# Kernel optimization log

Hardware: AMD Instinct MI355X
Metric: run time of the kernel (lower is better)

The kernel has to match this reference:

```python
import jax, jax.numpy as jnp
import numpy as np

B, N, V = 8, 2000, 2000
K = 100            # local_size
EMB = 128          # ff_hidden_dim
PENALTY = -1e9
EPS = 1e-5         # InstanceNorm eps


def setup_inputs() -> dict:
    key = jax.random.key(0)
    ks = jax.random.split(key, 16)
    s = 0.02
    return {
        "dist": jax.random.uniform(ks[0], (B, N, V), dtype=jnp.float32),
        "theta": jax.random.normal(ks[1], (B, N, V), dtype=jnp.float32),
        "scale": jax.random.uniform(ks[2], (B, N, 1), dtype=jnp.float32),
        # Linear params stored [in, out]
        "w1": jax.random.normal(ks[3], (2 * K + 1, EMB), dtype=jnp.float32) * s,
        "b1": jnp.zeros((EMB,), jnp.float32),
        "w2": jax.random.normal(ks[4], (EMB, 2 * EMB), dtype=jnp.float32) * s,
        "b2": jnp.zeros((2 * EMB,), jnp.float32),
        "w3": jax.random.normal(ks[5], (2 * EMB, EMB), dtype=jnp.float32) * s,
        "b3": jnp.zeros((EMB,), jnp.float32),
        "w4": jax.random.normal(ks[6], (EMB, K), dtype=jnp.float32) * s,
        "b4": jnp.zeros((K,), jnp.float32),
        "gamma": jnp.ones((2 * EMB,), jnp.float32),   # InstanceNorm affine weight
        "beta": jnp.zeros((2 * EMB,), jnp.float32),   # InstanceNorm affine bias
    }


def reference(dist, theta, scale, w1, b1, w2, b2, w3, b3, w4, b4, gamma, beta):
    # --- topk smallest distances (ascending) + gather theta ---
    neg_vals, idx = jax.lax.top_k(-dist, K)          # [B,N,K]
    sorted_dist = -neg_vals                           # ascending k smallest
    sorted_dist = sorted_dist / jnp.max(sorted_dist, axis=-1, keepdims=True)
    sorted_theta = jnp.take_along_axis(theta, idx, axis=-1)  # [B,N,K]

    # --- small MLP with InstanceNorm over the node dim ---
    x_in = jnp.concatenate([sorted_dist, sorted_theta, scale], axis=-1)  # [B,N,2K+1]
    emb = jax.nn.relu(x_in @ w1 + b1)                 # [B,N,EMB]
    h = jax.nn.relu(emb @ w2 + b2)                    # [B,N,2*EMB]
    # InstanceNorm1d: normalize each channel over the length (node) dim, biased var
    mean = jnp.mean(h, axis=1, keepdims=True)
    var = jnp.var(h, axis=1, keepdims=True)
    h = (h - mean) * jax.lax.rsqrt(var + EPS) * gamma + beta
    emb = jax.nn.relu(h @ w3 + b3)                    # [B,N,EMB]
    out = (emb @ w4 + b4) - sorted_dist               # [B,N,K]

    # --- scatter into penalty-initialized matrix ---
    out_mat = jnp.full((B, N, V), PENALTY, dtype=dist.dtype)
    b_ix = jnp.arange(B)[:, None, None]
    n_ix = jnp.arange(N)[None, :, None]
    return out_mat.at[b_ix, n_ix, idx].set(out)
```

## Files before the change

### kernel.cpp

```cpp
#include <hip/hip_runtime.h>
#include <hip/hip_bf16.h>

#define BB 8
#define NN 2000
#define VV 2000
#define KK 100
#define EMB 128
#define PENALTY -1e9f
#define NBIN 512
#define BINSCALE 2048.0f
#define CAP 200
#define XPAD 224
#define SMALLTHR (255.0f / 2048.0f)
#define NWPACK 212
#define TOPKB (BB * NN / 4)

typedef __attribute__((ext_vector_type(8))) short short8;
typedef __attribute__((ext_vector_type(4))) float f32x4;

#define WB() __builtin_amdgcn_wave_barrier()

__device__ __forceinline__ unsigned short bf16rne(float f) {
    unsigned u = __float_as_uint(f);
    u += 0x7FFF + ((u >> 16) & 1);
    return (unsigned short)(u >> 16);
}
__device__ __forceinline__ float bf2f(unsigned short s) {
    return __uint_as_float((unsigned)s << 16);
}

#define FORALL_VALS(BODY)                                                    \
    _Pragma("unroll") for (int ci = 0; ci < 8; ++ci) {                       \
        { const int j = 0; const float fv = v4[ci].x; const int e = (ci * 64 + lane) * 4 + 0; BODY } \
        { const int j = 1; const float fv = v4[ci].y; const int e = (ci * 64 + lane) * 4 + 1; BODY } \
        { const int j = 2; const float fv = v4[ci].z; const int e = (ci * 64 + lane) * 4 + 2; BODY } \
        { const int j = 3; const float fv = v4[ci].w; const int e = (ci * 64 + lane) * 4 + 3; BODY } \
    }

__global__ __launch_bounds__(256) void topk_kernel(
    const float* __restrict__ dist, const float* __restrict__ scale,
    unsigned short* __restrict__ xin, unsigned short* __restrict__ sdist,
    unsigned short* __restrict__ idxb,
    const float* __restrict__ w1, const float* __restrict__ w2,
    const float* __restrict__ w3, const float* __restrict__ w4,
    unsigned short* __restrict__ pw1, unsigned short* __restrict__ pw2,
    unsigned short* __restrict__ pw3, unsigned short* __restrict__ pw4)
{
    __shared__ __align__(16) unsigned hist[4][NBIN / 2];
    __shared__ __align__(16) unsigned snap[4][NBIN / 2];
    __shared__ unsigned long long comp[4][CAP];
    __shared__ unsigned long long comp2[4][KK];
    __shared__ int sh_cnt[4], sh_ntie[4], sh_kth[4];
    __shared__ unsigned sh_pref[4];
    __shared__ int sh_tie[4][64];

    const int t = threadIdx.x;

    if (blockIdx.x < NWPACK) {
        const int bt = blockIdx.x;
        for (int e = t; e < 512; e += 256) {
            int lane = e >> 3, j = e & 7;
            int kk = ((lane >> 4) << 3) + j;
            int nn = lane & 15;
            if (bt < 56) {
                int kt = bt >> 3, nt = bt & 7;
                int k = kt * 32 + kk, n = nt * 16 + nn;
                float f = (k < 201) ? w1[k * 128 + n] : 0.f;
                pw1[bt * 512 + e] = bf16rne(f);
            } else if (bt < 120) {
                int bb = bt - 56, kt = bb >> 4, nt = bb & 15;
                pw2[bb * 512 + e] = bf16rne(w2[(kt * 32 + kk) * 256 + nt * 16 + nn]);
            } else if (bt < 184) {
                int bb = bt - 120, kt = bb >> 3, nt = bb & 7;
                pw3[bb * 512 + e] = bf16rne(w3[(kt * 32 + kk) * 128 + nt * 16 + nn]);
            } else {
                int bb = bt - 184, kt = bb / 7, nt = bb % 7;
                int n = nt * 16 + nn;
                float f = (n < 100) ? w4[(kt * 32 + kk) * 100 + n] : 0.f;
                pw4[bb * 512 + e] = bf16rne(f);
            }
        }
        return;
    }

    const int w = t >> 6, lane = t & 63;
    const int row = (blockIdx.x - NWPACK) * 4 + w;
    const float4* d4 = (const float4*)(dist + (size_t)row * VV);

    float4 v4[8];
#pragma unroll
    for (int c = 0; c < 7; ++c) v4[c] = d4[c * 64 + lane];
    v4[7] = (lane < 52) ? d4[448 + lane] : make_float4(2.f, 2.f, 2.f, 2.f);

    int nsmall = 0;
    FORALL_VALS({ nsmall += (fv < SMALLTHR) ? 1 : 0; (void)e; (void)j; (void)ci; });
#pragma unroll
    for (int off = 1; off < 64; off <<= 1) nsmall += __shfl_xor(nsmall, off);
    const bool fast = (nsmall >= KK);

#pragma unroll
    for (int i = 0; i < 4; ++i) hist[w][lane * 4 + i] = 0u;
    if (lane == 0) { sh_cnt[w] = 0; sh_ntie[w] = 0; }
    WB();

    unsigned bcache[8];
    FORALL_VALS({
        int b = (int)(fv * BINSCALE);
        b = b < 0 ? 0 : (b > NBIN - 1 ? NBIN - 1 : b);
        int bb = b > 255 ? 255 : b;
        if (j == 0) bcache[ci] = (unsigned)bb;
        else bcache[ci] |= (unsigned)bb << (8 * j);
        bool doh = fast ? (b < 255) : (b < NBIN - 1);
        if (doh) atomicAdd(&hist[w][b >> 1], 1u << ((b & 1) << 4));
        (void)e;
    });
    WB();

    unsigned cw0 = hist[w][lane * 4 + 0];
    unsigned cw1 = hist[w][lane * 4 + 1];
    unsigned cw2 = hist[w][lane * 4 + 2];
    unsigned cw3 = hist[w][lane * 4 + 3];
    unsigned tot = (cw0 & 0xFFFFu) + (cw0 >> 16) + (cw1 & 0xFFFFu) + (cw1 >> 16) +
                   (cw2 & 0xFFFFu) + (cw2 >> 16) + (cw3 & 0xFFFFu) + (cw3 >> 16);
    unsigned incl = tot;
#pragma unroll
    for (int off = 1; off < 64; off <<= 1) {
        unsigned v = __shfl_up(incl, (unsigned)off);
        if (lane >= off) incl += v;
    }
    unsigned run = incl - tot;

    int myBt = -1, myM = 0;
#pragma unroll
    for (int i = 0; i < 4; ++i) {
        unsigned cwi = (i == 0) ? cw0 : (i == 1) ? cw1 : (i == 2) ? cw2 : cw3;
        unsigned c0 = cwi & 0xFFFFu, c1 = cwi >> 16;
        unsigned st0 = run, st1 = run + c0;
        if (myBt < 0 && st0 < KK && st0 + c0 >= KK) {
            myBt = lane * 8 + 2 * i; myM = (int)(st0 + c0);
        }
        if (myBt < 0 && st1 < KK && st1 + c1 >= KK) {
            myBt = lane * 8 + 2 * i + 1; myM = (int)(st1 + c1);
        }
        unsigned packed = st0 | (st1 << 16);
        hist[w][lane * 4 + i] = packed;
        snap[w][lane * 4 + i] = packed;
        run = st1 + c1;
    }
    WB();

    unsigned long long bl = __ballot(myBt >= 0);
    int Bt, m;
    if (bl != 0ull) {
        int src = __ffsll(bl) - 1;
        Bt = __shfl(myBt, src);
        m = __shfl(myM, src);
    } else {
        Bt = NBIN - 1;
        m = 100000;
    }

    if (m <= CAP) {
        FORALL_VALS({
            int b;
            if (fast) b = (int)((bcache[ci] >> (8 * j)) & 255u);
            else {
                b = (int)(fv * BINSCALE);
                b = b < 0 ? 0 : (b > NBIN - 1 ? NBIN - 1 : b);
            }
            if (b <= Bt) {
                int sh = (b & 1) << 4;
                unsigned old = atomicAdd(&hist[w][b >> 1], 1u << sh);
                int slot = (int)((old >> sh) & 0xFFFFu);
                comp[w][slot] =
                    ((unsigned long long)__float_as_uint(fv) << 32) | (unsigned)e;
            }
        });
        WB();
        for (int o = lane; o < m; o += 64) {
            unsigned long long key = comp[w][o];
            float fv = __uint_as_float((unsigned)(key >> 32));
            int b = (int)(fv * BINSCALE);
            b = b < 0 ? 0 : (b > NBIN - 1 ? NBIN - 1 : b);
            int sh = (b & 1) << 4;
            unsigned e0 = (hist[w][b >> 1] >> sh) & 0xFFFFu;
            unsigned s0 = (snap[w][b >> 1] >> sh) & 0xFFFFu;
            int r = (int)s0;
            for (unsigned s = s0; s < e0; ++s) r += (comp[w][s] < key);
            if (r < KK) comp2[w][r] = key;
        }
    } else {
        FORALL_VALS({
            int b = (int)(fv * BINSCALE);
            b = b < 0 ? 0 : (b > NBIN - 1 ? NBIN - 1 : b);
            if (b < Bt) {
                int pos = atomicAdd(&sh_cnt[w], 1);
                if (pos < CAP)
                    comp[w][pos] =
                        ((unsigned long long)__float_as_uint(fv) << 32) | (unsigned)e;
            }
            (void)j; (void)ci;
        });
        WB();
        int nless = sh_cnt[w];
        if (lane == 0) { sh_pref[w] = 0u; sh_kth[w] = KK - nless; }
        WB();
        for (int p = 0; p < 4; ++p) {
#pragma unroll
            for (int i = 0; i < 4; ++i) hist[w][lane * 4 + i] = 0u;
            WB();
            const int shift = 24 - 8 * p;
            const unsigned pref = sh_pref[w];
            FORALL_VALS({
                int b = (int)(fv * BINSCALE);
                b = b < 0 ? 0 : (b > NBIN - 1 ? NBIN - 1 : b);
                if (b == Bt) {
                    unsigned k = __float_as_uint(fv);
                    bool ok = (p == 0) || ((k >> (shift + 8)) == pref);
                    if (ok) atomicAdd(&hist[w][(k >> shift) & 255u], 1u);
                }
                (void)e; (void)j; (void)ci;
            });
            WB();
            if (lane == 0) {
                int kth = sh_kth[w];
                unsigned cum = 0;
                int b = 0;
                for (; b < 256; ++b) {
                    unsigned cc = hist[w][b];
                    if (cum + cc >= (unsigned)kth) break;
                    cum += cc;
                }
                sh_pref[w] = (pref << 8) | (unsigned)b;
                sh_kth[w] = kth - (int)cum;
            }
            WB();
        }
        const unsigned T = sh_pref[w];
        const int need2 = sh_kth[w];
        FORALL_VALS({
            int b = (int)(fv * BINSCALE);
            b = b < 0 ? 0 : (b > NBIN - 1 ? NBIN - 1 : b);
            if (b == Bt) {
                unsigned k = __float_as_uint(fv);
                if (k < T) {
                    int pos = atomicAdd(&sh_cnt[w], 1);
                    if (pos < CAP)
                        comp[w][pos] = ((unsigned long long)k << 32) | (unsigned)e;
                } else if (k == T) {
                    int q = atomicAdd(&sh_ntie[w], 1);
                    if (q < 64) sh_tie[w][q] = e;
                }
            }
            (void)j; (void)ci;
        });
        WB();
        if (lane == 0) {
            int nl2 = sh_cnt[w];
            int nt = sh_ntie[w] < 64 ? sh_ntie[w] : 64;
            for (int i = 1; i < nt; ++i) {
                int v = sh_tie[w][i], j2 = i - 1;
                while (j2 >= 0 && sh_tie[w][j2] > v) {
                    sh_tie[w][j2 + 1] = sh_tie[w][j2];
                    --j2;
                }
                sh_tie[w][j2 + 1] = v;
            }
            for (int i = 0; i < need2; ++i)
                comp[w][nl2 + i] =
                    ((unsigned long long)T << 32) | (unsigned)sh_tie[w][i];
            sh_cnt[w] = nl2 + need2;
        }
        WB();
        const int mm = sh_cnt[w];
        for (int o = lane; o < mm; o += 64) {
            unsigned long long key = comp[w][o];
            int r = 0;
            for (int j2 = 0; j2 < mm; ++j2) {
                unsigned long long cj = comp[w][j2];
                r += (cj < key) || (cj == key && j2 < o);
            }
            if (r < KK) comp2[w][r] = key;
        }
    }
    WB();

    const float Tf = __uint_as_float((unsigned)(comp2[w][KK - 1] >> 32));
    const float invT = 1.0f / Tf;
    for (int o = lane; o < KK; o += 64) {
        unsigned long long c = comp2[w][o];
        unsigned kbits = (unsigned)(c >> 32);
        int id = (int)(c & 0xFFFFFFFFu);
        unsigned short nb = bf16rne(__uint_as_float(kbits) * invT);
        xin[(size_t)row * XPAD + o] = nb;
        sdist[(size_t)row * KK + o] = nb;
        idxb[(size_t)row * KK + o] = (unsigned short)id;
    }
    if (lane == 0) xin[(size_t)row * XPAD + 200] = bf16rne(scale[row]);
    else if (lane < 24) xin[(size_t)row * XPAD + 200 + lane] = 0;
}

__global__ __launch_bounds__(256) void gather_kernel(
    const float* __restrict__ theta, const unsigned short* __restrict__ idxb,
    unsigned short* __restrict__ xin)
{
    const int i = blockIdx.x * 256 + threadIdx.x;
    const int row = i / KK;
    const int k = i - row * KK;
    const int id = (int)idxb[i];
    float v = theta[(size_t)row * VV + id];
    xin[(size_t)row * XPAD + 100 + k] = bf16rne(v);
}

__global__ __launch_bounds__(256) void fused12_mfma(
    const unsigned short* __restrict__ xin, const unsigned short* __restrict__ pw1,
    const float* __restrict__ b1, const unsigned short* __restrict__ pw2,
    const float* __restrict__ b2, unsigned short* __restrict__ h)
{
    __shared__ unsigned short c1s[64][136];
    const int t = threadIdx.x;
    const int w = t >> 6, l = t & 63;
    const int m0 = blockIdx.x * 64;
    const int lr = l & 15, lg = l >> 4;

    f32x4 acc[8] = {};
    const short8* arow = (const short8*)(xin + (size_t)(m0 + 16 * w + lr) * XPAD);
    const short8* pw1v = (const short8*)pw1;
#pragma unroll
    for (int kt = 0; kt < 7; ++kt) {
        short8 a = arow[kt * 4 + lg];
#pragma unroll
        for (int nt = 0; nt < 8; ++nt) {
            short8 b = pw1v[(kt * 8 + nt) * 64 + l];
            acc[nt] = __builtin_amdgcn_mfma_f32_16x16x32_bf16(a, b, acc[nt], 0, 0, 0);
        }
    }
#pragma unroll
    for (int nt = 0; nt < 8; ++nt) {
        int col = nt * 16 + lr;
        float bb = b1[col];
#pragma unroll
        for (int r = 0; r < 4; ++r) {
            float v = fmaxf(acc[nt][r] + bb, 0.f);
            c1s[16 * w + lg * 4 + r][col] = bf16rne(v);
        }
    }
    __syncthreads();

    f32x4 acc2[16] = {};
    const short8* pw2v = (const short8*)pw2;
#pragma unroll
    for (int kt = 0; kt < 4; ++kt) {
        short8 a = *(const short8*)&c1s[16 * w + lr][kt * 32 + lg * 8];
#pragma unroll
        for (int nt = 0; nt < 16; ++nt) {
            short8 b = pw2v[(kt * 16 + nt) * 64 + l];
            acc2[nt] = __builtin_amdgcn_mfma_f32_16x16x32_bf16(a, b, acc2[nt], 0, 0, 0);
        }
    }
#pragma unroll
    for (int nt = 0; nt < 16; ++nt) {
        int col = nt * 16 + lr;
        float bb = b2[col];
#pragma unroll
        for (int r = 0; r < 4; ++r) {
            float v = fmaxf(acc2[nt][r] + bb, 0.f);
            h[(size_t)(m0 + 16 * w + lg * 4 + r) * 256 + col] = bf16rne(v);
        }
    }
}

#define NCHUNK 25
#define CHUNK (NN / NCHUNK)

__global__ __launch_bounds__(256) void stats_partial(
    const unsigned short* __restrict__ h, float* __restrict__ part)
{
    const int b = blockIdx.x, ch = blockIdx.y, c = threadIdx.x;
    const unsigned short* base = h + ((size_t)b * NN + (size_t)ch * CHUNK) * 256 + c;
    float s = 0.f, s2 = 0.f;
    for (int n = 0; n < CHUNK; ++n) {
        float v = bf2f(base[(size_t)n * 256]);
        s += v;
        s2 += v * v;
    }
    size_t o = (((size_t)b * NCHUNK + ch) * 256 + c) * 2;
    part[o] = s;
    part[o + 1] = s2;
}

__global__ __launch_bounds__(256) void stats_final(
    const float* __restrict__ part, const float* __restrict__ gamma,
    const float* __restrict__ beta, float* __restrict__ scv,
    float* __restrict__ shv)
{
    const int b = blockIdx.x, c = threadIdx.x;
    float s = 0.f, s2 = 0.f;
    for (int ch = 0; ch < NCHUNK; ++ch) {
        size_t o = (((size_t)b * NCHUNK + ch) * 256 + c) * 2;
        s += part[o];
        s2 += part[o + 1];
    }
    const float inv = 1.0f / (float)NN;
    float mean = s * inv;
    float var = s2 * inv - mean * mean;
    float rs = rsqrtf(var + 1e-5f);
    float sc = gamma[c] * rs;
    scv[b * 256 + c] = sc;
    shv[b * 256 + c] = beta[c] - mean * sc;
}

__global__ __launch_bounds__(256) void fused34_mfma(
    const unsigned short* __restrict__ h, const unsigned short* __restrict__ pw3,
    const float* __restrict__ b3, const unsigned short* __restrict__ pw4,
    const float* __restrict__ b4, const float* __restrict__ scv,
    const float* __restrict__ shv, const unsigned short* __restrict__ sdist,
    const unsigned short* __restrict__ idxb, float* __restrict__ out)
{
    __shared__ __align__(16) char uni[64 * 100 * 4];
    __shared__ __align__(16) unsigned bm[64][64];
    __shared__ __align__(16) unsigned short wpref[64][64];
    unsigned short (*c1s)[136] = (unsigned short (*)[136])uni;
    float (*valbuf)[100] = (float (*)[100])uni;

    const int t = threadIdx.x;
    const int w = t >> 6, l = t & 63;
    const int m0 = blockIdx.x * 64;
    const int lr = l & 15, lg = l >> 4;

    for (int i = t; i < 64 * 64; i += 256) ((unsigned*)bm)[i] = 0u;
    __syncthreads();

    for (int i = t; i < 64 * KK; i += 256) {
        int rrow = i / KK;
        int id = (int)idxb[(size_t)(m0 + rrow) * KK + (i - rrow * KK)];
        atomicOr(&bm[rrow][id >> 5], 1u << (id & 31));
    }

    const int myrow = m0 + 16 * w + lr;
    const int mybatch = myrow / NN;

    f32x4 acc[8] = {};
    const short8* hrow = (const short8*)(h + (size_t)myrow * 256);
    const short8* pw3v = (const short8*)pw3;
#pragma unroll
    for (int kt = 0; kt < 8; ++kt) {
        int k0 = kt * 32 + lg * 8;
        short8 hv = hrow[kt * 4 + lg];
        const float4* scp = (const float4*)(scv + mybatch * 256 + k0);
        const float4* shp = (const float4*)(shv + mybatch * 256 + k0);
        float4 sc0 = scp[0], sc1 = scp[1];
        float4 sh0 = shp[0], sh1 = shp[1];
        short8 a;
        a[0] = (short)bf16rne(fmaf(bf2f((unsigned short)hv[0]), sc0.x, sh0.x));
        a[1] = (short)bf16rne(fmaf(bf2f((unsigned short)hv[1]), sc0.y, sh0.y));
        a[2] = (short)bf16rne(fmaf(bf2f((unsigned short)hv[2]), sc0.z, sh0.z));
        a[3] = (short)bf16rne(fmaf(bf2f((unsigned short)hv[3]), sc0.w, sh0.w));
        a[4] = (short)bf16rne(fmaf(bf2f((unsigned short)hv[4]), sc1.x, sh1.x));
        a[5] = (short)bf16rne(fmaf(bf2f((unsigned short)hv[5]), sc1.y, sh1.y));
        a[6] = (short)bf16rne(fmaf(bf2f((unsigned short)hv[6]), sc1.z, sh1.z));
        a[7] = (short)bf16rne(fmaf(bf2f((unsigned short)hv[7]), sc1.w, sh1.w));
#pragma unroll
        for (int nt = 0; nt < 8; ++nt) {
            short8 b = pw3v[(kt * 8 + nt) * 64 + l];
            acc[nt] = __builtin_amdgcn_mfma_f32_16x16x32_bf16(a, b, acc[nt], 0, 0, 0);
        }
    }
    __syncthreads();

    if (t < 64) {
        unsigned run = 0;
#pragma unroll
        for (int wd = 0; wd < 63; ++wd) {
            wpref[t][wd] = (unsigned short)run;
            run += (unsigned)__popc(bm[t][wd]);
        }
        wpref[t][63] = (unsigned short)run;
    }

#pragma unroll
    for (int nt = 0; nt < 8; ++nt) {
        int col = nt * 16 + lr;
        float bb = b3[col];
#pragma unroll
        for (int r = 0; r < 4; ++r) {
            float v = fmaxf(acc[nt][r] + bb, 0.f);
            c1s[16 * w + lg * 4 + r][col] = bf16rne(v);
        }
    }
    __syncthreads();

    f32x4 acc2[7] = {};
    const short8* pw4v = (const short8*)pw4;
#pragma unroll
    for (int kt = 0; kt < 4; ++kt) {
        short8 a = *(const short8*)&c1s[16 * w + lr][kt * 32 + lg * 8];
#pragma unroll
        for (int nt = 0; nt < 7; ++nt) {
            short8 b = pw4v[(kt * 7 + nt) * 64 + l];
            acc2[nt] = __builtin_amdgcn_mfma_f32_16x16x32_bf16(a, b, acc2[nt], 0, 0, 0);
        }
    }
    __syncthreads();

#pragma unroll
    for (int nt = 0; nt < 7; ++nt) {
        int col = nt * 16 + lr;
        if (col < KK) {
            float bb = b4[col];
#pragma unroll
            for (int r = 0; r < 4; ++r) {
                int r4 = 16 * w + lg * 4 + r;
                int mrow = m0 + r4;
                float v = acc2[nt][r] + bb -
                          bf2f(sdist[(size_t)mrow * KK + col]);
                int id = (int)idxb[(size_t)mrow * KK + col];
                int wd = id >> 5;
                int irank = (int)wpref[r4][wd] +
                            __popc(bm[r4][wd] & ((1u << (id & 31)) - 1u));
                valbuf[r4][irank] = v;
            }
        }
    }
    __syncthreads();

    for (int i = t; i < 64 * (VV / 4); i += 256) {
        int rrow = i / (VV / 4);
        int p = i - rrow * (VV / 4);
        int v0 = p * 4;
        unsigned word = bm[rrow][v0 >> 5];
        int sh = v0 & 31;
        int racc = (int)wpref[rrow][v0 >> 5] + __popc(word & ((1u << sh) - 1u));
        float4 o;
        unsigned b0 = (word >> sh) & 1u;
        o.x = b0 ? valbuf[rrow][racc] : PENALTY; racc += b0;
        unsigned b1_ = (word >> (sh + 1)) & 1u;
        o.y = b1_ ? valbuf[rrow][racc] : PENALTY; racc += b1_;
        unsigned b2_ = (word >> (sh + 2)) & 1u;
        o.z = b2_ ? valbuf[rrow][racc] : PENALTY; racc += b2_;
        unsigned b3_ = (word >> (sh + 3)) & 1u;
        o.w = b3_ ? valbuf[rrow][racc] : PENALTY;
        ((float4*)(out + (size_t)(m0 + rrow) * VV))[p] = o;
    }
}

extern "C" void kernel_launch(void* const* d_in, const int* in_sizes, int n_in,
                              void* d_out, int out_size, void* d_ws, size_t ws_size,
                              hipStream_t stream)
{
    const float* dist  = (const float*)d_in[0];
    const float* theta = (const float*)d_in[1];
    const float* scale = (const float*)d_in[2];
    const float* w1 = (const float*)d_in[3];
    const float* b1 = (const float*)d_in[4];
    const float* w2 = (const float*)d_in[5];
    const float* b2 = (const float*)d_in[6];
    const float* w3 = (const float*)d_in[7];
    const float* b3 = (const float*)d_in[8];
    const float* w4 = (const float*)d_in[9];
    const float* b4 = (const float*)d_in[10];
    const float* gamma = (const float*)d_in[11];
    const float* beta  = (const float*)d_in[12];
    float* out = (float*)d_out;

    const int M = BB * NN;

    char* p = (char*)d_ws;
    unsigned short* xin   = (unsigned short*)p;     p += (size_t)M * XPAD * 2;
    unsigned short* h     = (unsigned short*)p;     p += (size_t)M * 256 * 2;
    unsigned short* sdist = (unsigned short*)p;     p += (size_t)M * KK * 2;
    unsigned short* idxb  = (unsigned short*)p;     p += (size_t)M * KK * 2;
    float* part  = (float*)p;                       p += (size_t)BB * NCHUNK * 256 * 2 * 4;
    float* scv   = (float*)p;                       p += 8 * 256 * 4;
    float* shv   = (float*)p;                       p += 8 * 256 * 4;
    unsigned short* pw1 = (unsigned short*)p;       p += 56 * 512 * 2;
    unsigned short* pw2 = (unsigned short*)p;       p += 64 * 512 * 2;
    unsigned short* pw3 = (unsigned short*)p;       p += 64 * 512 * 2;
    unsigned short* pw4 = (unsigned short*)p;       p += 28 * 512 * 2;

    topk_kernel<<<NWPACK + TOPKB, 256, 0, stream>>>(
        dist, scale, xin, sdist, idxb,
        w1, w2, w3, w4, pw1, pw2, pw3, pw4);

    gather_kernel<<<(M * KK) / 256, 256, 0, stream>>>(theta, idxb, xin);

    fused12_mfma<<<M / 64, 256, 0, stream>>>(xin, pw1, b1, pw2, b2, h);

    stats_partial<<<dim3(BB, NCHUNK), 256, 0, stream>>>(h, part);
    stats_final<<<BB, 256, 0, stream>>>(part, gamma, beta, scv, shv);

    fused34_mfma<<<M / 64, 256, 0, stream>>>(h, pw3, b3, pw4, b4, scv, shv,
                                             sdist, idxb, out);
}
```

Baseline: 133.8 us.

## Split each top-k row across two waves with block-level synchronization

The top-k selection kernel now assigns two wavefronts per row (two rows per block) instead of one wave per row. This halves the per-thread register footprint of the distance values and doubles the number of blocks. The cost is that wave barriers become full __syncthreads and the histogram is built via atomics from two waves. The fallback path is now taken by both rows together if either needs it, and the prefix scan runs on only half the threads.

```diff
diff --git a/kernel.cpp b/kernel.cpp
--- a/kernel.cpp
+++ b/kernel.cpp
@@ -13,12 +13,10 @@
 #define XPAD 224
 #define SMALLTHR (255.0f / 2048.0f)
 #define NWPACK 212
-#define TOPKB (BB * NN / 4)
+#define TOPKB (BB * NN / 2)
 
 typedef __attribute__((ext_vector_type(8))) short short8;
 typedef __attribute__((ext_vector_type(4))) float f32x4;
-
-#define WB() __builtin_amdgcn_wave_barrier()
 
 __device__ __forceinline__ unsigned short bf16rne(float f) {
     unsigned u = __float_as_uint(f);
@@ -29,12 +27,12 @@
     return __uint_as_float((unsigned)s << 16);
 }
 
-#define FORALL_VALS(BODY)                                                    \
-    _Pragma("unroll") for (int ci = 0; ci < 8; ++ci) {                       \
-        { const int j = 0; const float fv = v4[ci].x; const int e = (ci * 64 + lane) * 4 + 0; BODY } \
-        { const int j = 1; const float fv = v4[ci].y; const int e = (ci * 64 + lane) * 4 + 1; BODY } \
-        { const int j = 2; const float fv = v4[ci].z; const int e = (ci * 64 + lane) * 4 + 2; BODY } \
-        { const int j = 3; const float fv = v4[ci].w; const int e = (ci * 64 + lane) * 4 + 3; BODY } \
+#define FORALL16(BODY)                                                       \
+    _Pragma("unroll") for (int ci = 0; ci < 4; ++ci) {                       \
+        { const int j = 0; const float fv = v4[ci].x; const int e = (ci * 128 + hl) * 4 + 0; BODY } \
+        { const int j = 1; const float fv = v4[ci].y; const int e = (ci * 128 + hl) * 4 + 1; BODY } \
+        { const int j = 2; const float fv = v4[ci].z; const int e = (ci * 128 + hl) * 4 + 2; BODY } \
+        { const int j = 3; const float fv = v4[ci].w; const int e = (ci * 128 + hl) * 4 + 3; BODY } \
     }
 
 __global__ __launch_bounds__(256) void topk_kernel(
@@ -46,13 +44,15 @@
     unsigned short* __restrict__ pw1, unsigned short* __restrict__ pw2,
     unsigned short* __restrict__ pw3, unsigned short* __restrict__ pw4)
 {
-    __shared__ __align__(16) unsigned hist[4][NBIN / 2];
-    __shared__ __align__(16) unsigned snap[4][NBIN / 2];
-    __shared__ unsigned long long comp[4][CAP];
-    __shared__ unsigned long long comp2[4][KK];
-    __shared__ int sh_cnt[4], sh_ntie[4], sh_kth[4];
-    __shared__ unsigned sh_pref[4];
-    __shared__ int sh_tie[4][64];
+    __shared__ __align__(16) unsigned hist[2][NBIN / 2];
+    __shared__ __align__(16) unsigned snap[2][NBIN / 2];
+    __shared__ unsigned long long comp[2][CAP];
+    __shared__ unsigned long long comp2[2][KK];
+    __shared__ int sh_ns[2][2];
+    __shared__ int sh_Bt[2], sh_m[2];
+    __shared__ int sh_cnt[2], sh_ntie[2], sh_kth[2];
+    __shared__ unsigned sh_pref[2];
+    __shared__ int sh_tie[2][64];
 
     const int t = threadIdx.x;
 
@@ -84,84 +84,90 @@
     }
 
     const int w = t >> 6, lane = t & 63;
-    const int row = (blockIdx.x - NWPACK) * 4 + w;
+    const int wr = w >> 1;
+    const int half = w & 1;
+    const int hl = (half << 6) | lane;
+    const int row = (blockIdx.x - NWPACK) * 2 + wr;
     const float4* d4 = (const float4*)(dist + (size_t)row * VV);
 
-    float4 v4[8];
-#pragma unroll
-    for (int c = 0; c < 7; ++c) v4[c] = d4[c * 64 + lane];
-    v4[7] = (lane < 52) ? d4[448 + lane] : make_float4(2.f, 2.f, 2.f, 2.f);
+    float4 v4[4];
+#pragma unroll
+    for (int c = 0; c < 4; ++c) {
+        int i4 = c * 128 + hl;
+        v4[c] = (i4 < VV / 4) ? d4[i4] : make_float4(2.f, 2.f, 2.f, 2.f);
+    }
 
     int nsmall = 0;
-    FORALL_VALS({ nsmall += (fv < SMALLTHR) ? 1 : 0; (void)e; (void)j; (void)ci; });
-#pragma unroll
-    for (int off = 1; off < 64; off <<= 1) nsmall += __shfl_xor(nsmall, off);
-    const bool fast = (nsmall >= KK);
-
-#pragma unroll
-    for (int i = 0; i < 4; ++i) hist[w][lane * 4 + i] = 0u;
-    if (lane == 0) { sh_cnt[w] = 0; sh_ntie[w] = 0; }
-    WB();
-
-    unsigned bcache[8];
-    FORALL_VALS({
+    unsigned bcache[4];
+    FORALL16({
         int b = (int)(fv * BINSCALE);
         b = b < 0 ? 0 : (b > NBIN - 1 ? NBIN - 1 : b);
         int bb = b > 255 ? 255 : b;
         if (j == 0) bcache[ci] = (unsigned)bb;
         else bcache[ci] |= (unsigned)bb << (8 * j);
-        bool doh = fast ? (b < 255) : (b < NBIN - 1);
-        if (doh) atomicAdd(&hist[w][b >> 1], 1u << ((b & 1) << 4));
+        nsmall += (fv < SMALLTHR) ? 1 : 0;
         (void)e;
     });
-    WB();
-
-    unsigned cw0 = hist[w][lane * 4 + 0];
-    unsigned cw1 = hist[w][lane * 4 + 1];
-    unsigned cw2 = hist[w][lane * 4 + 2];
-    unsigned cw3 = hist[w][lane * 4 + 3];
-    unsigned tot = (cw0 & 0xFFFFu) + (cw0 >> 16) + (cw1 & 0xFFFFu) + (cw1 >> 16) +
-                   (cw2 & 0xFFFFu) + (cw2 >> 16) + (cw3 & 0xFFFFu) + (cw3 >> 16);
-    unsigned incl = tot;
-#pragma unroll
-    for (int off = 1; off < 64; off <<= 1) {
-        unsigned v = __shfl_up(incl, (unsigned)off);
-        if (lane >= off) incl += v;
-    }
-    unsigned run = incl - tot;
-
-    int myBt = -1, myM = 0;
-#pragma unroll
-    for (int i = 0; i < 4; ++i) {
-        unsigned cwi = (i == 0) ? cw0 : (i == 1) ? cw1 : (i == 2) ? cw2 : cw3;
-        unsigned c0 = cwi & 0xFFFFu, c1 = cwi >> 16;
-        unsigned st0 = run, st1 = run + c0;
-        if (myBt < 0 && st0 < KK && st0 + c0 >= KK) {
-            myBt = lane * 8 + 2 * i; myM = (int)(st0 + c0);
-        }
-        if (myBt < 0 && st1 < KK && st1 + c1 >= KK) {
-            myBt = lane * 8 + 2 * i + 1; myM = (int)(st1 + c1);
-        }
-        unsigned packed = st0 | (st1 << 16);
-        hist[w][lane * 4 + i] = packed;
-        snap[w][lane * 4 + i] = packed;
-        run = st1 + c1;
-    }
-    WB();
-
-    unsigned long long bl = __ballot(myBt >= 0);
-    int Bt, m;
-    if (bl != 0ull) {
-        int src = __ffsll(bl) - 1;
-        Bt = __shfl(myBt, src);
-        m = __shfl(myM, src);
-    } else {
-        Bt = NBIN - 1;
-        m = 100000;
-    }
-
-    if (m <= CAP) {
-        FORALL_VALS({
+#pragma unroll
+    for (int off = 1; off < 64; off <<= 1) nsmall += __shfl_xor(nsmall, off);
+
+    ((unsigned*)hist)[t] = 0u;
+    ((unsigned*)hist)[t + 256] = 0u;
+    if (lane == 0) sh_ns[wr][half] = nsmall;
+    if (t < 2) { sh_Bt[t] = NBIN - 1; sh_m[t] = 100000; sh_cnt[t] = 0; sh_ntie[t] = 0; }
+    __syncthreads();
+    const bool fast = (sh_ns[wr][0] + sh_ns[wr][1] >= KK);
+
+    FORALL16({
+        int b = (int)(fv * BINSCALE);
+        b = b < 0 ? 0 : (b > NBIN - 1 ? NBIN - 1 : b);
+        bool doh = fast ? (b < 255) : (b < NBIN - 1);
+        if (doh) atomicAdd(&hist[wr][b >> 1], 1u << ((b & 1) << 4));
+        (void)e; (void)j; (void)ci;
+    });
+    __syncthreads();
+
+    if (half == 0) {
+        unsigned cw0 = hist[wr][lane * 4 + 0];
+        unsigned cw1 = hist[wr][lane * 4 + 1];
+        unsigned cw2 = hist[wr][lane * 4 + 2];
+        unsigned cw3 = hist[wr][lane * 4 + 3];
+        unsigned tot = (cw0 & 0xFFFFu) + (cw0 >> 16) + (cw1 & 0xFFFFu) + (cw1 >> 16) +
+                       (cw2 & 0xFFFFu) + (cw2 >> 16) + (cw3 & 0xFFFFu) + (cw3 >> 16);
+        unsigned incl = tot;
+#pragma unroll
+        for (int off = 1; off < 64; off <<= 1) {
+            unsigned v = __shfl_up(incl, (unsigned)off);
+            if (lane >= off) incl += v;
+        }
+        unsigned run = incl - tot;
+
+        int myBt = -1, myM = 0;
+#pragma unroll
+        for (int i = 0; i < 4; ++i) {
+            unsigned cwi = (i == 0) ? cw0 : (i == 1) ? cw1 : (i == 2) ? cw2 : cw3;
+            unsigned c0 = cwi & 0xFFFFu, c1 = cwi >> 16;
+            unsigned st0 = run, st1 = run + c0;
+            if (myBt < 0 && st0 < KK && st0 + c0 >= KK) {
+                myBt = lane * 8 + 2 * i; myM = (int)(st0 + c0);
+            }
+            if (myBt < 0 && st1 < KK && st1 + c1 >= KK) {
+                myBt = lane * 8 + 2 * i + 1; myM = (int)(st1 + c1);
+            }
+            unsigned packed = st0 | (st1 << 16);
+            hist[wr][lane * 4 + i] = packed;
+            snap[wr][lane * 4 + i] = packed;
+            run = st1 + c1;
+        }
+        if (myBt >= 0) { sh_Bt[wr] = myBt; sh_m[wr] = myM; }
+    }
+    __syncthreads();
+    const int Bt = sh_Bt[wr];
+    const int m = sh_m[wr];
+    const bool anyfb = (sh_m[0] > CAP) || (sh_m[1] > CAP);
+
+    if (!anyfb) {
+        FORALL16({
             int b;
             if (fast) b = (int)((bcache[ci] >> (8 * j)) & 255u);
             else {
@@ -170,134 +176,134 @@
             }
             if (b <= Bt) {
                 int sh = (b & 1) << 4;
-                unsigned old = atomicAdd(&hist[w][b >> 1], 1u << sh);
+                unsigned old = atomicAdd(&hist[wr][b >> 1], 1u << sh);
                 int slot = (int)((old >> sh) & 0xFFFFu);
-                comp[w][slot] =
+                comp[wr][slot] =
                     ((unsigned long long)__float_as_uint(fv) << 32) | (unsigned)e;
             }
         });
-        WB();
-        for (int o = lane; o < m; o += 64) {
-            unsigned long long key = comp[w][o];
+        __syncthreads();
+        for (int o = hl; o < m; o += 128) {
+            unsigned long long key = comp[wr][o];
             float fv = __uint_as_float((unsigned)(key >> 32));
             int b = (int)(fv * BINSCALE);
             b = b < 0 ? 0 : (b > NBIN - 1 ? NBIN - 1 : b);
             int sh = (b & 1) << 4;
-            unsigned e0 = (hist[w][b >> 1] >> sh) & 0xFFFFu;
-            unsigned s0 = (snap[w][b >> 1] >> sh) & 0xFFFFu;
+            unsigned e0 = (hist[wr][b >> 1] >> sh) & 0xFFFFu;
+            unsigned s0 = (snap[wr][b >> 1] >> sh) & 0xFFFFu;
             int r = (int)s0;
-            for (unsigned s = s0; s < e0; ++s) r += (comp[w][s] < key);
-            if (r < KK) comp2[w][r] = key;
+            for (unsigned s = s0; s < e0; ++s) r += (comp[wr][s] < key);
+            if (r < KK) comp2[wr][r] = key;
         }
     } else {
-        FORALL_VALS({
+        FORALL16({
             int b = (int)(fv * BINSCALE);
             b = b < 0 ? 0 : (b > NBIN - 1 ? NBIN - 1 : b);
             if (b < Bt) {
-                int pos = atomicAdd(&sh_cnt[w], 1);
+                int pos = atomicAdd(&sh_cnt[wr], 1);
                 if (pos < CAP)
-                    comp[w][pos] =
+                    comp[wr][pos] =
                         ((unsigned long long)__float_as_uint(fv) << 32) | (unsigned)e;
             }
             (void)j; (void)ci;
         });
-        WB();
-        int nless = sh_cnt[w];
-        if (lane == 0) { sh_pref[w] = 0u; sh_kth[w] = KK - nless; }
-        WB();
+        __syncthreads();
+        int nless = sh_cnt[wr];
+        if (hl == 0) { sh_pref[wr] = 0u; sh_kth[wr] = KK - nless; }
+        __syncthreads();
         for (int p = 0; p < 4; ++p) {
-#pragma unroll
-            for (int i = 0; i < 4; ++i) hist[w][lane * 4 + i] = 0u;
-            WB();
+            hist[wr][hl] = 0u;
+            hist[wr][hl + 128] = 0u;
+            __syncthreads();
             const int shift = 24 - 8 * p;
-            const unsigned pref = sh_pref[w];
-            FORALL_VALS({
+            const unsigned pref = sh_pref[wr];
+            FORALL16({
                 int b = (int)(fv * BINSCALE);
                 b = b < 0 ? 0 : (b > NBIN - 1 ? NBIN - 1 : b);
                 if (b == Bt) {
                     unsigned k = __float_as_uint(fv);
                     bool ok = (p == 0) || ((k >> (shift + 8)) == pref);
-                    if (ok) atomicAdd(&hist[w][(k >> shift) & 255u], 1u);
+                    if (ok) atomicAdd(&hist[wr][(k >> shift) & 255u], 1u);
                 }
                 (void)e; (void)j; (void)ci;
             });
-            WB();
-            if (lane == 0) {
-                int kth = sh_kth[w];
+            __syncthreads();
+            if (hl == 0) {
+                int kth = sh_kth[wr];
                 unsigned cum = 0;
                 int b = 0;
                 for (; b < 256; ++b) {
-                    unsigned cc = hist[w][b];
+                    unsigned cc = hist[wr][b];
                     if (cum + cc >= (unsigned)kth) break;
                     cum += cc;
                 }
-                sh_pref[w] = (pref << 8) | (unsigned)b;
-                sh_kth[w] = kth - (int)cum;
-            }
-            WB();
-        }
-        const unsigned T = sh_pref[w];
-        const int need2 = sh_kth[w];
-        FORALL_VALS({
+                sh_pref[wr] = (pref << 8) | (unsigned)b;
+                sh_kth[wr] = kth - (int)cum;
+            }
+            __syncthreads();
+        }
+        const unsigned T = sh_pref[wr];
+        const int need2 = sh_kth[wr];
+        FORALL16({
             int b = (int)(fv * BINSCALE);
             b = b < 0 ? 0 : (b > NBIN - 1 ? NBIN - 1 : b);
             if (b == Bt) {
                 unsigned k = __float_as_uint(fv);
                 if (k < T) {
-                    int pos = atomicAdd(&sh_cnt[w], 1);
+                    int pos = atomicAdd(&sh_cnt[wr], 1);
                     if (pos < CAP)
-                        comp[w][pos] = ((unsigned long long)k << 32) | (unsigned)e;
+                        comp[wr][pos] = ((unsigned long long)k << 32) | (unsigned)e;
                 } else if (k == T) {
-                    int q = atomicAdd(&sh_ntie[w], 1);
-                    if (q < 64) sh_tie[w][q] = e;
+                    int q = atomicAdd(&sh_ntie[wr], 1);
+                    if (q < 64) sh_tie[wr][q] = e;
                 }
             }
             (void)j; (void)ci;
         });
-        WB();
-        if (lane == 0) {
-            int nl2 = sh_cnt[w];
-            int nt = sh_ntie[w] < 64 ? sh_ntie[w] : 64;
+        __syncthreads();
+        if (hl == 0) {
+            int nl2 = sh_cnt[wr];
+            int nt = sh_ntie[wr] < 64 ? sh_ntie[wr] : 64;
             for (int i = 1; i < nt; ++i) {
-                int v = sh_tie[w][i], j2 = i - 1;
-                while (j2 >= 0 && sh_tie[w][j2] > v) {
-                    sh_tie[w][j2 + 1] = sh_tie[w][j2];
+                int v = sh_tie[wr][i], j2 = i - 1;
+                while (j2 >= 0 && sh_tie[wr][j2] > v) {
+                    sh_tie[wr][j2 + 1] = sh_tie[wr][j2];
                     --j2;
                 }
-                sh_tie[w][j2 + 1] = v;
+                sh_tie[wr][j2 + 1] = v;
             }
             for (int i = 0; i < need2; ++i)
-                comp[w][nl2 + i] =
-                    ((unsigned long long)T << 32) | (unsigned)sh_tie[w][i];
-            sh_cnt[w] = nl2 + need2;
-        }
-        WB();
-        const int mm = sh_cnt[w];
-        for (int o = lane; o < mm; o += 64) {
-            unsigned long long key = comp[w][o];
+                comp[wr][nl2 + i] =
+                    ((unsigned long long)T << 32) | (unsigned)sh_tie[wr][i];
+            sh_cnt[wr] = nl2 + need2;
+        }
+        __syncthreads();
+        const int mm = sh_cnt[wr];
+        for (int o = hl; o < mm; o += 128) {
+            unsigned long long key = comp[wr][o];
             int r = 0;
             for (int j2 = 0; j2 < mm; ++j2) {
-                unsigned long long cj = comp[w][j2];
+                unsigned long long cj = comp[wr][j2];
                 r += (cj < key) || (cj == key && j2 < o);
             }
-            if (r < KK) comp2[w][r] = key;
-        }
-    }
-    WB();
-
-    const float Tf = __uint_as_float((unsigned)(comp2[w][KK - 1] >> 32));
+            if (r < KK) comp2[wr][r] = key;
+        }
+    }
+    __syncthreads();
+
+    const float Tf = __uint_as_float((unsigned)(comp2[wr][KK - 1] >> 32));
     const float invT = 1.0f / Tf;
-    for (int o = lane; o < KK; o += 64) {
-        unsigned long long c = comp2[w][o];
+    if (hl < KK) {
+        unsigned long long c = comp2[wr][hl];
         unsigned kbits = (unsigned)(c >> 32);
         int id = (int)(c & 0xFFFFFFFFu);
         unsigned short nb = bf16rne(__uint_as_float(kbits) * invT);
-        xin[(size_t)row * XPAD + o] = nb;
-        sdist[(size_t)row * KK + o] = nb;
-        idxb[(size_t)row * KK + o] = (unsigned short)id;
-    }
-    if (lane == 0) xin[(size_t)row * XPAD + 200] = bf16rne(scale[row]);
-    else if (lane < 24) xin[(size_t)row * XPAD + 200 + lane] = 0;
+        xin[(size_t)row * XPAD + hl] = nb;
+        sdist[(size_t)row * KK + hl] = nb;
+        idxb[(size_t)row * KK + hl] = (unsigned short)id;
+    }
+    if (hl == 0) xin[(size_t)row * XPAD + 200] = bf16rne(scale[row]);
+    else if (hl < 24) xin[(size_t)row * XPAD + 200 + hl] = 0;
 }
 
 __global__ __launch_bounds__(256) void gather_kernel(
```

Result: slower. 136.6 us (+2.1%).

## Fuse InstanceNorm statistics into layer-2 epilogue and finalize in layer-3 kernel

Applied to the files above, without the earlier changes.

Each fused12 block reduces its tile's per-channel sum and sum of squares in shared memory. It then atomically adds them into a small per-batch global buffer, which is zeroed by the topk kernel. This removes the stats_partial and stats_final launches and the re-read of h. fused34 now computes scale and shift from the raw sums at block start, handling tiles that straddle a batch boundary. In exchange it adds float atomics, which make the accumulation order nondeterministic, plus some redundant per-block rsqrt work.

```diff
diff --git a/kernel.cpp b/kernel.cpp
--- a/kernel.cpp
+++ b/kernel.cpp
@@ -44,7 +44,8 @@
     const float* __restrict__ w1, const float* __restrict__ w2,
     const float* __restrict__ w3, const float* __restrict__ w4,
     unsigned short* __restrict__ pw1, unsigned short* __restrict__ pw2,
-    unsigned short* __restrict__ pw3, unsigned short* __restrict__ pw4)
+    unsigned short* __restrict__ pw3, unsigned short* __restrict__ pw4,
+    float* __restrict__ part)
 {
     __shared__ __align__(16) unsigned hist[4][NBIN / 2];
     __shared__ __align__(16) unsigned snap[4][NBIN / 2];
@@ -58,6 +59,10 @@
 
     if (blockIdx.x < NWPACK) {
         const int bt = blockIdx.x;
+        if (bt == 0) {
+#pragma unroll
+            for (int i = 0; i < 16; ++i) part[i * 256 + t] = 0.f;
+        }
         for (int e = t; e < 512; e += 256) {
             int lane = e >> 3, j = e & 7;
             int kk = ((lane >> 4) << 3) + j;
@@ -315,9 +320,10 @@
 __global__ __launch_bounds__(256) void fused12_mfma(
     const unsigned short* __restrict__ xin, const unsigned short* __restrict__ pw1,
     const float* __restrict__ b1, const unsigned short* __restrict__ pw2,
-    const float* __restrict__ b2, unsigned short* __restrict__ h)
+    const float* __restrict__ b2, unsigned short* __restrict__ h,
+    float* __restrict__ part)
 {
-    __shared__ unsigned short c1s[64][136];
+    __shared__ __align__(16) unsigned short c1s[64][136];
     const int t = threadIdx.x;
     const int w = t >> 6, l = t & 63;
     const int m0 = blockIdx.x * 64;
@@ -358,63 +364,49 @@
             acc2[nt] = __builtin_amdgcn_mfma_f32_16x16x32_bf16(a, b, acc2[nt], 0, 0, 0);
         }
     }
+    __syncthreads();
+    float* sums = (float*)c1s;
+    for (int i = t; i < 1024; i += 256) sums[i] = 0.f;
+    __syncthreads();
+
+    const int batch0 = m0 / NN;
+    const int bl = ((m0 + 16 * w + lg * 4) / NN) - batch0;
 #pragma unroll
     for (int nt = 0; nt < 16; ++nt) {
         int col = nt * 16 + lr;
         float bb = b2[col];
+        float s = 0.f, s2 = 0.f;
 #pragma unroll
         for (int r = 0; r < 4; ++r) {
             float v = fmaxf(acc2[nt][r] + bb, 0.f);
             h[(size_t)(m0 + 16 * w + lg * 4 + r) * 256 + col] = bf16rne(v);
-        }
-    }
-}
-
-#define NCHUNK 25
-#define CHUNK (NN / NCHUNK)
-
-__global__ __launch_bounds__(256) void stats_partial(
-    const unsigned short* __restrict__ h, float* __restrict__ part)
-{
-    const int b = blockIdx.x, ch = blockIdx.y, c = threadIdx.x;
-    const unsigned short* base = h + ((size_t)b * NN + (size_t)ch * CHUNK) * 256 + c;
-    float s = 0.f, s2 = 0.f;
-    for (int n = 0; n < CHUNK; ++n) {
-        float v = bf2f(base[(size_t)n * 256]);
-        s += v;
-        s2 += v * v;
-    }
-    size_t o = (((size_t)b * NCHUNK + ch) * 256 + c) * 2;
-    part[o] = s;
-    part[o + 1] = s2;
-}
-
-__global__ __launch_bounds__(256) void stats_final(
-    const float* __restrict__ part, const float* __restrict__ gamma,
-    const float* __restrict__ beta, float* __restrict__ scv,
-    float* __restrict__ shv)
-{
-    const int b = blockIdx.x, c = threadIdx.x;
-    float s = 0.f, s2 = 0.f;
-    for (int ch = 0; ch < NCHUNK; ++ch) {
-        size_t o = (((size_t)b * NCHUNK + ch) * 256 + c) * 2;
-        s += part[o];
-        s2 += part[o + 1];
-    }
-    const float inv = 1.0f / (float)NN;
-    float mean = s * inv;
-    float var = s2 * inv - mean * mean;
-    float rs = rsqrtf(var + 1e-5f);
-    float sc = gamma[c] * rs;
-    scv[b * 256 + c] = sc;
-    shv[b * 256 + c] = beta[c] - mean * sc;
+            s += v;
+            s2 += v * v;
+        }
+        atomicAdd(&sums[(bl * 256 + col) * 2 + 0], s);
+        atomicAdd(&sums[(bl * 256 + col) * 2 + 1], s2);
+    }
+    __syncthreads();
+    {
+        const int col = t;
+        const bool strad = ((m0 + 63) / NN) != batch0;
+        atomicAdd(&part[(batch0 * 256 + col) * 2 + 0], sums[col * 2 + 0]);
+        atomicAdd(&part[(batch0 * 256 + col) * 2 + 1], sums[col * 2 + 1]);
+        if (strad) {
+            atomicAdd(&part[((batch0 + 1) * 256 + col) * 2 + 0],
+                      sums[(256 + col) * 2 + 0]);
+            atomicAdd(&part[((batch0 + 1) * 256 + col) * 2 + 1],
+                      sums[(256 + col) * 2 + 1]);
+        }
+    }
 }
 
 __global__ __launch_bounds__(256) void fused34_mfma(
     const unsigned short* __restrict__ h, const unsigned short* __restrict__ pw3,
     const float* __restrict__ b3, const unsigned short* __restrict__ pw4,
-    const float* __restrict__ b4, const float* __restrict__ scv,
-    const float* __restrict__ shv, const unsigned short* __restrict__ sdist,
+    const float* __restrict__ b4, const float* __restrict__ part,
+    const float* __restrict__ gamma, const float* __restrict__ beta,
+    const unsigned short* __restrict__ sdist,
     const unsigned short* __restrict__ idxb, float* __restrict__ out)
 {
     __shared__ __align__(16) char uni[64 * 100 * 4];
@@ -422,11 +414,36 @@
     __shared__ __align__(16) unsigned short wpref[64][64];
     unsigned short (*c1s)[136] = (unsigned short (*)[136])uni;
     float (*valbuf)[100] = (float (*)[100])uni;
+    float* scl = (float*)wpref;
+    float* shl = scl + 512;
 
     const int t = threadIdx.x;
     const int w = t >> 6, l = t & 63;
     const int m0 = blockIdx.x * 64;
     const int lr = l & 15, lg = l >> 4;
+    const int batch0 = m0 / NN;
+    const bool strad = ((m0 + 63) / NN) != batch0;
+
+    {
+        const int col = t;
+        float g = gamma[col], be = beta[col];
+        float s = part[(batch0 * 256 + col) * 2 + 0];
+        float s2 = part[(batch0 * 256 + col) * 2 + 1];
+        float mean = s * (1.0f / NN);
+        float var = s2 * (1.0f / NN) - mean * mean;
+        float sc = g * rsqrtf(var + 1e-5f);
+        scl[col] = sc;
+        shl[col] = be - mean * sc;
+        if (strad) {
+            s = part[((batch0 + 1) * 256 + col) * 2 + 0];
+            s2 = part[((batch0 + 1) * 256 + col) * 2 + 1];
+            mean = s * (1.0f / NN);
+            var = s2 * (1.0f / NN) - mean * mean;
+            sc = g * rsqrtf(var + 1e-5f);
+            scl[256 + col] = sc;
+            shl[256 + col] = be - mean * sc;
+        }
+    }
 
     for (int i = t; i < 64 * 64; i += 256) ((unsigned*)bm)[i] = 0u;
     __syncthreads();
@@ -438,7 +455,8 @@
     }
 
     const int myrow = m0 + 16 * w + lr;
-    const int mybatch = myrow / NN;
+    const int bl = (myrow / NN) - batch0;
+    const int nbase = bl * 256;
 
     f32x4 acc[8] = {};
     const short8* hrow = (const short8*)(h + (size_t)myrow * 256);
@@ -447,19 +465,11 @@
     for (int kt = 0; kt < 8; ++kt) {
         int k0 = kt * 32 + lg * 8;
         short8 hv = hrow[kt * 4 + lg];
-        const float4* scp = (const float4*)(scv + mybatch * 256 + k0);
-        const float4* shp = (const float4*)(shv + mybatch * 256 + k0);
-        float4 sc0 = scp[0], sc1 = scp[1];
-        float4 sh0 = shp[0], sh1 = shp[1];
         short8 a;
-        a[0] = (short)bf16rne(fmaf(bf2f((unsigned short)hv[0]), sc0.x, sh0.x));
-        a[1] = (short)bf16rne(fmaf(bf2f((unsigned short)hv[1]), sc0.y, sh0.y));
-        a[2] = (short)bf16rne(fmaf(bf2f((unsigned short)hv[2]), sc0.z, sh0.z));
-        a[3] = (short)bf16rne(fmaf(bf2f((unsigned short)hv[3]), sc0.w, sh0.w));
-        a[4] = (short)bf16rne(fmaf(bf2f((unsigned short)hv[4]), sc1.x, sh1.x));
-        a[5] = (short)bf16rne(fmaf(bf2f((unsigned short)hv[5]), sc1.y, sh1.y));
-        a[6] = (short)bf16rne(fmaf(bf2f((unsigned short)hv[6]), sc1.z, sh1.z));
-        a[7] = (short)bf16rne(fmaf(bf2f((unsigned short)hv[7]), sc1.w, sh1.w));
+#pragma unroll
+        for (int i = 0; i < 8; ++i)
+            a[i] = (short)bf16rne(fmaf(bf2f((unsigned short)hv[i]),
+                                       scl[nbase + k0 + i], shl[nbase + k0 + i]));
 #pragma unroll
         for (int nt = 0; nt < 8; ++nt) {
             short8 b = pw3v[(kt * 8 + nt) * 64 + l];
@@ -570,9 +580,7 @@
     unsigned short* h     = (unsigned short*)p;     p += (size_t)M * 256 * 2;
     unsigned short* sdist = (unsigned short*)p;     p += (size_t)M * KK * 2;
     unsigned short* idxb  = (unsigned short*)p;     p += (size_t)M * KK * 2;
-    float* part  = (float*)p;                       p += (size_t)BB * NCHUNK * 256 * 2 * 4;
-    float* scv   = (float*)p;                       p += 8 * 256 * 4;
-    float* shv   = (float*)p;                       p += 8 * 256 * 4;
+    float* part  = (float*)p;                       p += 8 * 256 * 2 * 4;
     unsigned short* pw1 = (unsigned short*)p;       p += 56 * 512 * 2;
     unsigned short* pw2 = (unsigned short*)p;       p += 64 * 512 * 2;
     unsigned short* pw3 = (unsigned short*)p;       p += 64 * 512 * 2;
@@ -580,15 +588,12 @@
 
     topk_kernel<<<NWPACK + TOPKB, 256, 0, stream>>>(
         dist, scale, xin, sdist, idxb,
-        w1, w2, w3, w4, pw1, pw2, pw3, pw4);
+        w1, w2, w3, w4, pw1, pw2, pw3, pw4, part);
 
     gather_kernel<<<(M * KK) / 256, 256, 0, stream>>>(theta, idxb, xin);
 
-    fused12_mfma<<<M / 64, 256, 0, stream>>>(xin, pw1, b1, pw2, b2, h);
-
-    stats_partial<<<dim3(BB, NCHUNK), 256, 0, stream>>>(h, part);
-    stats_final<<<BB, 256, 0, stream>>>(part, gamma, beta, scv, shv);
-
-    fused34_mfma<<<M / 64, 256, 0, stream>>>(h, pw3, b3, pw4, b4, scv, shv,
-                                             sdist, idxb, out);
-}
+    fused12_mfma<<<M / 64, 256, 0, stream>>>(xin, pw1, b1, pw2, b2, h, part);
+
+    fused34_mfma<<<M / 64, 256, 0, stream>>>(h, pw3, b3, pw4, b4, part,
+                                             gamma, beta, sdist, idxb, out);
+}
```

Measured after the change: 143.0 us. 1.07x slower.
